# Kernel optimization log

Measured on AMD Instinct MI355X. Metric: run time of the kernel, lower is better.

## Reference

```python
import jax, jax.numpy as jnp
import numpy as np

N = 100_000      # nodes
E = 1_600_000    # edges (avg degree 16)
IN, H, C = 32, 32, 8


def setup_inputs() -> dict:
    key = jax.random.key(0)
    k0, k1, k2, k3, k4 = jax.random.split(key, 5)
    in_feat = jax.random.normal(k0, (N, IN), jnp.float32)
    src = jax.random.randint(k1, (E,), 0, N, dtype=jnp.int32)
    dst = jax.random.randint(k2, (E,), 0, N, dtype=jnp.int32)
    # Glorot-ish init for the two GraphConv weights, zero bias (DGL default)
    W1 = jax.random.normal(k3, (IN, H), jnp.float32) * (1.0 / np.sqrt(IN))
    b1 = jnp.zeros((H,), jnp.float32)
    W2 = jax.random.normal(k4, (H, C), jnp.float32) * (1.0 / np.sqrt(H))
    b2 = jnp.zeros((C,), jnp.float32)
    return {"in_feat": in_feat, "src": src, "dst": dst,
            "W1": W1, "b1": b1, "W2": W2, "b2": b2}


def _graph_conv(x, src, dst, W, b):
    """DGL GraphConv, norm='both': D_in^{-1/2} A D_out^{-1/2} (x W) + b."""
    ones = jnp.ones((src.shape[0],), x.dtype)
    deg_out = jnp.clip(jax.ops.segment_sum(ones, src, num_segments=N), 1.0)  # [N]
    deg_in = jnp.clip(jax.ops.segment_sum(ones, dst, num_segments=N), 1.0)   # [N]
    # weight applied before aggregation (DGL does this when in>=out; same math)
    h = (x @ W) * jax.lax.rsqrt(deg_out)[:, None]                # [N, out]
    agg = jax.ops.segment_sum(h[src], dst, num_segments=N)       # gather + scatter-add
    return agg * jax.lax.rsqrt(deg_in)[:, None] + b


def reference(in_feat, src, dst, W1, b1, W2, b2):
    h = jax.nn.relu(_graph_conv(in_feat, src, dst, W1, b1))
    h = _graph_conv(h, src, dst, W2, b2)
    return jnp.mean(h, axis=0)  # mean-pool readout over all nodes -> [C]
```

## Files before the change

kernel.cpp:

```cpp
#include <hip/hip_runtime.h>
#include <hip/hip_fp16.h>

#define NN 100000
#define NE 1600000
#define INF 32
#define HF 32
#define CF 8

#define SH1 11
#define BN1 2048
#define NB1 49
#define CAP1 36864
#define BNODE 64
#define NBF (NB1 * 32)
#define CAPF 1280
#define CHUNK 2048
#define NBLK_BIN ((NE + CHUNK - 1) / CHUNK)

__global__ void zero_kernel(uint4* __restrict__ p, int n16) {
    int i = blockIdx.x * blockDim.x + threadIdx.x;
    if (i < n16) p[i] = make_uint4(0u, 0u, 0u, 0u);
}

__global__ void __launch_bounds__(256) bin_coarse_kernel(
        const int* __restrict__ src, const int* __restrict__ dst,
        int* __restrict__ gcur_d, int* __restrict__ gcur_s,
        unsigned int* __restrict__ bins_d, unsigned int* __restrict__ bins_s) {
    __shared__ int cnt_d[4][NB1], base_d[4][NB1], cnt_s[4][NB1], base_s[4][NB1];
    const int tid = threadIdx.x;
    const int w = tid >> 6;
    for (int i = tid; i < 4 * NB1; i += 256) {
        (&cnt_d[0][0])[i] = 0; (&cnt_s[0][0])[i] = 0;
    }
    __syncthreads();
    int e0 = blockIdx.x * CHUNK;
    int e1 = min(e0 + CHUNK, NE);
    for (int e = e0 + tid; e < e1; e += 256) {
        atomicAdd(&cnt_d[w][dst[e] >> SH1], 1);
        atomicAdd(&cnt_s[w][src[e] >> SH1], 1);
    }
    __syncthreads();
    if (tid < NB1) {
        int c0 = cnt_d[0][tid], c1 = cnt_d[1][tid], c2 = cnt_d[2][tid], c3 = cnt_d[3][tid];
        int tot = c0 + c1 + c2 + c3;
        int b = tot ? atomicAdd(&gcur_d[tid], tot) : 0;
        base_d[0][tid] = b; base_d[1][tid] = b + c0;
        base_d[2][tid] = b + c0 + c1; base_d[3][tid] = b + c0 + c1 + c2;
        cnt_d[0][tid] = 0; cnt_d[1][tid] = 0; cnt_d[2][tid] = 0; cnt_d[3][tid] = 0;
        c0 = cnt_s[0][tid]; c1 = cnt_s[1][tid]; c2 = cnt_s[2][tid]; c3 = cnt_s[3][tid];
        tot = c0 + c1 + c2 + c3;
        b = tot ? atomicAdd(&gcur_s[tid], tot) : 0;
        base_s[0][tid] = b; base_s[1][tid] = b + c0;
        base_s[2][tid] = b + c0 + c1; base_s[3][tid] = b + c0 + c1 + c2;
        cnt_s[0][tid] = 0; cnt_s[1][tid] = 0; cnt_s[2][tid] = 0; cnt_s[3][tid] = 0;
    }
    __syncthreads();
    for (int e = e0 + tid; e < e1; e += 256) {
        int d = dst[e], s = src[e];
        int b = d >> SH1;
        int off = base_d[w][b] + atomicAdd(&cnt_d[w][b], 1);
        if (off < CAP1)
            bins_d[(size_t)b * CAP1 + off] = ((unsigned)(d & (BN1 - 1)) << 17) | (unsigned)s;
        b = s >> SH1;
        off = base_s[w][b] + atomicAdd(&cnt_s[w][b], 1);
        if (off < CAP1)
            bins_s[(size_t)b * CAP1 + off] = ((unsigned)(s & (BN1 - 1)) << 17) | (unsigned)d;
    }
}

__global__ void __launch_bounds__(256) bin_fine_kernel(
        const unsigned int* __restrict__ bins_d, const int* __restrict__ gcur_d,
        int* __restrict__ gcur_f, unsigned int* __restrict__ bins_f,
        int* __restrict__ deg_in) {
    __shared__ int cnt[8][32], base[8][32];
    __shared__ int ncnt[BN1];
    const int cb = blockIdx.x >> 4;
    const int sl = blockIdx.x & 15;
    const int tid = threadIdx.x;
    const int r = tid >> 5;
    (&cnt[0][0])[tid] = 0;
    for (int i = tid; i < BN1; i += 256) ncnt[i] = 0;
    __syncthreads();
    const int m = min(gcur_d[cb], CAP1);
    const int beg = (sl * m) >> 4;
    const int end = ((sl + 1) * m) >> 4;
    const unsigned int* bb = bins_d + (size_t)cb * CAP1;
    for (int j = beg + tid; j < end; j += 256) {
        int d10 = (int)(bb[j] >> 17);
        atomicAdd(&cnt[r][d10 >> 6], 1);
        atomicAdd(&ncnt[d10], 1);
    }
    __syncthreads();
    if (tid < 32) {
        int c[8], tot = 0;
        #pragma unroll
        for (int k = 0; k < 8; ++k) { c[k] = cnt[k][tid]; tot += c[k]; }
        int b = tot ? atomicAdd(&gcur_f[cb * 32 + tid], tot) : 0;
        #pragma unroll
        for (int k = 0; k < 8; ++k) { base[k][tid] = b; b += c[k]; cnt[k][tid] = 0; }
    }
    __syncthreads();
    for (int j = beg + tid; j < end; j += 256) {
        unsigned p = bb[j];
        int d10 = p >> 17;
        int f = d10 >> 6;
        int off = base[r][f] + atomicAdd(&cnt[r][f], 1);
        if (off < CAPF)
            bins_f[(size_t)(cb * 32 + f) * CAPF + off] =
                ((unsigned)(d10 & 63) << 17) | (p & 0x1FFFFu);
    }
    for (int i = tid; i < BN1; i += 256) {
        int c = ncnt[i];
        int n = cb * BN1 + i;
        if (c && n < NN) atomicAdd(&deg_in[n], c);
    }
}

__global__ void __launch_bounds__(256) srcside_kernel(
        const unsigned int* __restrict__ bins_s, const int* __restrict__ gcur_s,
        const int* __restrict__ deg_in,
        int* __restrict__ deg_out, float* __restrict__ wgt) {
    __shared__ int cnt[BN1];
    __shared__ float sw[BN1];
    const int cb = blockIdx.x >> 3;
    const int sl = blockIdx.x & 7;
    const int tid = threadIdx.x;
    for (int i = tid; i < BN1; i += 256) { cnt[i] = 0; sw[i] = 0.f; }
    __syncthreads();
    const int m = min(gcur_s[cb], CAP1);
    const int beg = (sl * m) >> 3;
    const int end = ((sl + 1) * m) >> 3;
    const unsigned int* bb = bins_s + (size_t)cb * CAP1;
    for (int j = beg + tid; j < end; j += 256) {
        unsigned p = bb[j];
        int local = p >> 17;
        int d = p & 0x1FFFF;
        float riv = rsqrtf(fmaxf((float)deg_in[d], 1.0f));
        atomicAdd(&cnt[local], 1);
        atomicAdd(&sw[local], riv);
    }
    __syncthreads();
    for (int i = tid; i < BN1; i += 256) {
        int c = cnt[i];
        int n = cb * BN1 + i;
        if (c && n < NN) {
            atomicAdd(&deg_out[n], c);
            atomicAdd(&wgt[n], sw[i]);
        }
    }
}

__global__ void xw1_kernel(const float* __restrict__ x, const float* __restrict__ W1,
                           const int* __restrict__ deg_out, unsigned int* __restrict__ h) {
    __shared__ float w[INF * HF];
    for (int i = threadIdx.x; i < INF * HF; i += blockDim.x) w[i] = W1[i];
    __syncthreads();
    int n = blockIdx.x * blockDim.x + threadIdx.x;
    if (n >= NN) return;

    float xr[INF];
    const float4* xp = (const float4*)(x + (size_t)n * INF);
    #pragma unroll
    for (int i = 0; i < INF / 4; ++i) {
        float4 v = xp[i];
        xr[4*i+0] = v.x; xr[4*i+1] = v.y; xr[4*i+2] = v.z; xr[4*i+3] = v.w;
    }
    float acc[HF];
    #pragma unroll
    for (int c = 0; c < HF; ++c) acc[c] = 0.0f;
    #pragma unroll
    for (int k = 0; k < INF; ++k) {
        float xv = xr[k];
        #pragma unroll
        for (int c = 0; c < HF; ++c) acc[c] = fmaf(xv, w[k * HF + c], acc[c]);
    }
    float rs = rsqrtf(fmaxf((float)deg_out[n], 1.0f));
    unsigned int pk[HF / 2];
    #pragma unroll
    for (int i = 0; i < HF / 2; ++i) {
        __half2 p = __floats2half2_rn(acc[2*i] * rs, acc[2*i+1] * rs);
        pk[i] = *(unsigned int*)&p;
    }
    uint4* hp = (uint4*)(h + (size_t)n * (HF / 2));
    #pragma unroll
    for (int i = 0; i < 4; ++i) {
        uint4 v;
        v.x = pk[4*i+0]; v.y = pk[4*i+1]; v.z = pk[4*i+2]; v.w = pk[4*i+3];
        hp[i] = v;
    }
}

__global__ void __launch_bounds__(256) gather_kernel(
        const unsigned int* __restrict__ bins, const int* __restrict__ gcur,
        const unsigned int* __restrict__ h, const int* __restrict__ deg_out,
        const float* __restrict__ wgt, const float* __restrict__ b1,
        float* __restrict__ v) {
    __shared__ int s_cnt[BNODE];
    __shared__ int s_start[BNODE];
    __shared__ int s_cur[BNODE];
    __shared__ int s_src[CAPF];
    __shared__ float vl[32];
    const int tid = threadIdx.x;
    const int b = blockIdx.x;
    const int m = min(gcur[b], CAPF);
    const unsigned int* bb = bins + (size_t)b * CAPF;

    if (tid < BNODE) s_cnt[tid] = 0;
    __syncthreads();
    for (int j = tid; j < m; j += 256) atomicAdd(&s_cnt[bb[j] >> 17], 1);
    __syncthreads();
    if (tid < 64) {
        int c = s_cnt[tid];
        int sc = c;
        #pragma unroll
        for (int off = 1; off < 64; off <<= 1) {
            int t = __shfl_up(sc, off, 64);
            if (tid >= off) sc += t;
        }
        s_start[tid] = sc - c;
        s_cur[tid] = sc - c;
    }
    __syncthreads();
    for (int j = tid; j < m; j += 256) {
        unsigned p = bb[j];
        int pos = atomicAdd(&s_cur[p >> 17], 1);
        s_src[pos] = (int)(p & 0x1FFFF);
    }
    __syncthreads();

    const int lane4 = tid & 3;
    const int g = tid >> 2;
    float b1r[8];
    #pragma unroll
    for (int c = 0; c < 8; ++c) b1r[c] = b1[lane4 * 8 + c];
    float vacc[8] = {0.f,0.f,0.f,0.f,0.f,0.f,0.f,0.f};

    #define ACC8(q) { float2 f0_ = __half22float2(*(__half2*)&(q).x); \
                      float2 f1_ = __half22float2(*(__half2*)&(q).y); \
                      float2 f2_ = __half22float2(*(__half2*)&(q).z); \
                      float2 f3_ = __half22float2(*(__half2*)&(q).w); \
                      a[0]+=f0_.x; a[1]+=f0_.y; a[2]+=f1_.x; a[3]+=f1_.y; \
                      a[4]+=f2_.x; a[5]+=f2_.y; a[6]+=f3_.x; a[7]+=f3_.y; }

    int n = b * BNODE + g;
    if (n < NN) {
        int beg = s_start[g];
        int cn = s_cnt[g];
        int end = beg + cn;
        float a[8] = {0.f,0.f,0.f,0.f,0.f,0.f,0.f,0.f};
        int j = beg;
        for (; j + 8 <= end; j += 8) {
            int t0 = s_src[j+0], t1 = s_src[j+1], t2 = s_src[j+2], t3 = s_src[j+3];
            int t4 = s_src[j+4], t5 = s_src[j+5], t6 = s_src[j+6], t7 = s_src[j+7];
            uint4 q0 = *(const uint4*)(h + (size_t)t0 * 16 + lane4 * 4);
            uint4 q1 = *(const uint4*)(h + (size_t)t1 * 16 + lane4 * 4);
            uint4 q2 = *(const uint4*)(h + (size_t)t2 * 16 + lane4 * 4);
            uint4 q3 = *(const uint4*)(h + (size_t)t3 * 16 + lane4 * 4);
            uint4 q4 = *(const uint4*)(h + (size_t)t4 * 16 + lane4 * 4);
            uint4 q5 = *(const uint4*)(h + (size_t)t5 * 16 + lane4 * 4);
            uint4 q6 = *(const uint4*)(h + (size_t)t6 * 16 + lane4 * 4);
            uint4 q7 = *(const uint4*)(h + (size_t)t7 * 16 + lane4 * 4);
            ACC8(q0) ACC8(q1) ACC8(q2) ACC8(q3)
            ACC8(q4) ACC8(q5) ACC8(q6) ACC8(q7)
        }
        for (; j + 4 <= end; j += 4) {
            int t0 = s_src[j+0], t1 = s_src[j+1], t2 = s_src[j+2], t3 = s_src[j+3];
            uint4 q0 = *(const uint4*)(h + (size_t)t0 * 16 + lane4 * 4);
            uint4 q1 = *(const uint4*)(h + (size_t)t1 * 16 + lane4 * 4);
            uint4 q2 = *(const uint4*)(h + (size_t)t2 * 16 + lane4 * 4);
            uint4 q3 = *(const uint4*)(h + (size_t)t3 * 16 + lane4 * 4);
            ACC8(q0) ACC8(q1) ACC8(q2) ACC8(q3)
        }
        for (; j < end; ++j) {
            int t0 = s_src[j];
            uint4 q0 = *(const uint4*)(h + (size_t)t0 * 16 + lane4 * 4);
            ACC8(q0)
        }
        float rs_in  = rsqrtf(fmaxf((float)cn, 1.0f));
        float rs_out = rsqrtf(fmaxf((float)deg_out[n], 1.0f));
        float alpha = rs_out * wgt[n];
        #pragma unroll
        for (int c = 0; c < 8; ++c)
            vacc[c] += alpha * fmaxf(fmaf(a[c], rs_in, b1r[c]), 0.f);
    }
    #undef ACC8

    #pragma unroll
    for (int c = 0; c < 8; ++c) {
        vacc[c] += __shfl_xor(vacc[c], 4, 64);
        vacc[c] += __shfl_xor(vacc[c], 8, 64);
        vacc[c] += __shfl_xor(vacc[c], 16, 64);
        vacc[c] += __shfl_xor(vacc[c], 32, 64);
    }
    if (tid < 32) vl[tid] = 0.f;
    __syncthreads();
    if ((tid & 63) < 4) {
        #pragma unroll
        for (int c = 0; c < 8; ++c) atomicAdd(&vl[lane4 * 8 + c], vacc[c]);
    }
    __syncthreads();
    if (tid < 32) atomicAdd(&v[tid], vl[tid]);
}

__global__ void final_kernel(const float* __restrict__ v, const float* __restrict__ W2,
                             const float* __restrict__ b2, float* __restrict__ out) {
    int c = threadIdx.x;
    if (c < CF) {
        float s = 0.f;
        #pragma unroll
        for (int k = 0; k < HF; ++k) s = fmaf(v[k], W2[k * CF + c], s);
        out[c] = s * (1.0f / NN) + b2[c];
    }
}

static inline size_t align256(size_t x) { return (x + 255) & ~(size_t)255; }

extern "C" void kernel_launch(void* const* d_in, const int* in_sizes, int n_in,
                              void* d_out, int out_size, void* d_ws, size_t ws_size,
                              hipStream_t stream) {
    const float* x   = (const float*)d_in[0];
    const int*   src = (const int*)  d_in[1];
    const int*   dst = (const int*)  d_in[2];
    const float* W1  = (const float*)d_in[3];
    const float* b1  = (const float*)d_in[4];
    const float* W2  = (const float*)d_in[5];
    const float* b2  = (const float*)d_in[6];
    float* out = (float*)d_out;

    char* base = (char*)d_ws;
    size_t off = 0;
    int*   gcur_d  = (int*)(base + off);   off = align256(off + NB1 * 4);
    int*   gcur_s  = (int*)(base + off);   off = align256(off + NB1 * 4);
    int*   gcur_f  = (int*)(base + off);   off = align256(off + NBF * 4);
    float* v       = (float*)(base + off); off = align256(off + 32 * 4);
    int*   deg_in  = (int*)(base + off);   off = align256(off + NN * 4);
    int*   deg_out = (int*)(base + off);   off = align256(off + NN * 4);
    float* wgt     = (float*)(base + off); off = align256(off + NN * 4);
    size_t zero_bytes = off;
    unsigned int* h      = (unsigned int*)(base + off); off = align256(off + (size_t)NN * 16 * 4);
    unsigned int* bins_d = (unsigned int*)(base + off); off = align256(off + (size_t)NB1 * CAP1 * 4);
    unsigned int* bins_s = (unsigned int*)(base + off); off = align256(off + (size_t)NB1 * CAP1 * 4);
    unsigned int* bins_f = (unsigned int*)(base + off); off = align256(off + (size_t)NBF * CAPF * 4);

    const int B = 256;
    int n16 = (int)(zero_bytes / 16);
    zero_kernel<<<(n16 + B - 1) / B, B, 0, stream>>>((uint4*)base, n16);

    bin_coarse_kernel<<<NBLK_BIN, B, 0, stream>>>(src, dst, gcur_d, gcur_s, bins_d, bins_s);
    bin_fine_kernel<<<NB1 * 16, B, 0, stream>>>(bins_d, gcur_d, gcur_f, bins_f, deg_in);
    srcside_kernel<<<NB1 * 8, B, 0, stream>>>(bins_s, gcur_s, deg_in, deg_out, wgt);
    xw1_kernel<<<(NN + B - 1) / B, B, 0, stream>>>(x, W1, deg_out, h);
    gather_kernel<<<NBF, B, 0, stream>>>(bins_f, gcur_f, h, deg_out, wgt, b1, v);
    final_kernel<<<1, 64, 0, stream>>>(v, W2, b2, out);
}
```

Before: 123.6 us.

## Fuse all pipeline stages into one cooperative persistent kernel with grid syncs

Merges the zero, binning, fine-binning, source-side degree, XW1, gather and final kernels into a single cooperative kernel launched with a persistent grid sized from occupancy. Each stage loops over its original block indices and stages are separated by grid-wide syncs. The aim is to remove the launch overhead and gaps between seven small kernels. In exchange, occupancy is limited by the shared-memory and register needs of the merged kernel, stages that had more blocks than the grid now loop, and grid syncs have their own cost. The old multi-kernel path remains as a fallback if the cooperative launch fails.

Result: no change. 123.8 us (+0.2%).

```diff
diff --git a/kernel.cpp b/kernel.cpp
--- a/kernel.cpp
+++ b/kernel.cpp
@@ -1,5 +1,7 @@
 #include <hip/hip_runtime.h>
 #include <hip/hip_fp16.h>
+#include <hip/hip_cooperative_groups.h>
+namespace cg = cooperative_groups;
 
 #define NN 100000
 #define NE 1600000
@@ -16,6 +18,313 @@
 #define CAPF 1280
 #define CHUNK 2048
 #define NBLK_BIN ((NE + CHUNK - 1) / CHUNK)
+
+#define SMEM_INTS 4096
+
+__global__ void __launch_bounds__(256) mega_kernel(
+        const float* __restrict__ x, const int* __restrict__ src, const int* __restrict__ dst,
+        const float* __restrict__ W1, const float* __restrict__ b1,
+        const float* __restrict__ W2, const float* __restrict__ b2,
+        float* __restrict__ out,
+        int* gcur_d, int* gcur_s, int* gcur_f, float* v,
+        int* deg_in, int* deg_out, float* wgt,
+        unsigned int* h, unsigned int* bins_d, unsigned int* bins_s, unsigned int* bins_f,
+        uint4* zbase, int n16) {
+    cg::grid_group gg = cg::this_grid();
+    __shared__ __align__(16) int smem[SMEM_INTS];
+    const int tid = threadIdx.x;
+    const int nb = gridDim.x;
+    const int gsz = nb * 256;
+
+    for (int i = blockIdx.x * 256 + tid; i < n16; i += gsz)
+        zbase[i] = make_uint4(0u, 0u, 0u, 0u);
+    __threadfence();
+    gg.sync();
+
+    {
+        int* cnt_d  = smem;
+        int* base_d = smem + 196;
+        int* cnt_s  = smem + 392;
+        int* base_s = smem + 588;
+        const int w = tid >> 6;
+        for (int c = blockIdx.x; c < NBLK_BIN; c += nb) {
+            for (int i = tid; i < 196; i += 256) { cnt_d[i] = 0; cnt_s[i] = 0; }
+            __syncthreads();
+            int e0 = c * CHUNK, e1 = min(e0 + CHUNK, NE);
+            for (int e = e0 + tid; e < e1; e += 256) {
+                atomicAdd(&cnt_d[w * 49 + (dst[e] >> SH1)], 1);
+                atomicAdd(&cnt_s[w * 49 + (src[e] >> SH1)], 1);
+            }
+            __syncthreads();
+            if (tid < NB1) {
+                int c0 = cnt_d[tid], c1 = cnt_d[49 + tid], c2 = cnt_d[98 + tid], c3 = cnt_d[147 + tid];
+                int tot = c0 + c1 + c2 + c3;
+                int b = tot ? atomicAdd(&gcur_d[tid], tot) : 0;
+                base_d[tid] = b; base_d[49 + tid] = b + c0;
+                base_d[98 + tid] = b + c0 + c1; base_d[147 + tid] = b + c0 + c1 + c2;
+                cnt_d[tid] = 0; cnt_d[49 + tid] = 0; cnt_d[98 + tid] = 0; cnt_d[147 + tid] = 0;
+                c0 = cnt_s[tid]; c1 = cnt_s[49 + tid]; c2 = cnt_s[98 + tid]; c3 = cnt_s[147 + tid];
+                tot = c0 + c1 + c2 + c3;
+                b = tot ? atomicAdd(&gcur_s[tid], tot) : 0;
+                base_s[tid] = b; base_s[49 + tid] = b + c0;
+                base_s[98 + tid] = b + c0 + c1; base_s[147 + tid] = b + c0 + c1 + c2;
+                cnt_s[tid] = 0; cnt_s[49 + tid] = 0; cnt_s[98 + tid] = 0; cnt_s[147 + tid] = 0;
+            }
+            __syncthreads();
+            for (int e = e0 + tid; e < e1; e += 256) {
+                int d = dst[e], s = src[e];
+                int b = d >> SH1;
+                int off = base_d[w * 49 + b] + atomicAdd(&cnt_d[w * 49 + b], 1);
+                if (off < CAP1)
+                    bins_d[(size_t)b * CAP1 + off] = ((unsigned)(d & (BN1 - 1)) << 17) | (unsigned)s;
+                b = s >> SH1;
+                off = base_s[w * 49 + b] + atomicAdd(&cnt_s[w * 49 + b], 1);
+                if (off < CAP1)
+                    bins_s[(size_t)b * CAP1 + off] = ((unsigned)(s & (BN1 - 1)) << 17) | (unsigned)d;
+            }
+            __syncthreads();
+        }
+    }
+    __threadfence();
+    gg.sync();
+
+    {
+        int* cnt  = smem;
+        int* base = smem + 256;
+        int* ncnt = smem + 512;
+        const int r = tid >> 5;
+        for (int t = blockIdx.x; t < NB1 * 16; t += nb) {
+            const int cb = t >> 4, sl = t & 15;
+            cnt[tid] = 0;
+            for (int i = tid; i < BN1; i += 256) ncnt[i] = 0;
+            __syncthreads();
+            const int m = min(gcur_d[cb], CAP1);
+            const int beg = (sl * m) >> 4, end = ((sl + 1) * m) >> 4;
+            const unsigned int* bb = bins_d + (size_t)cb * CAP1;
+            for (int j = beg + tid; j < end; j += 256) {
+                int d10 = (int)(bb[j] >> 17);
+                atomicAdd(&cnt[r * 32 + (d10 >> 6)], 1);
+                atomicAdd(&ncnt[d10], 1);
+            }
+            __syncthreads();
+            if (tid < 32) {
+                int cc[8], tot = 0;
+                #pragma unroll
+                for (int k = 0; k < 8; ++k) { cc[k] = cnt[k * 32 + tid]; tot += cc[k]; }
+                int b = tot ? atomicAdd(&gcur_f[cb * 32 + tid], tot) : 0;
+                #pragma unroll
+                for (int k = 0; k < 8; ++k) { base[k * 32 + tid] = b; b += cc[k]; cnt[k * 32 + tid] = 0; }
+            }
+            __syncthreads();
+            for (int j = beg + tid; j < end; j += 256) {
+                unsigned p = bb[j];
+                int d10 = p >> 17;
+                int f = d10 >> 6;
+                int off = base[r * 32 + f] + atomicAdd(&cnt[r * 32 + f], 1);
+                if (off < CAPF)
+                    bins_f[(size_t)(cb * 32 + f) * CAPF + off] =
+                        ((unsigned)(d10 & 63) << 17) | (p & 0x1FFFFu);
+            }
+            for (int i = tid; i < BN1; i += 256) {
+                int c = ncnt[i];
+                int n = cb * BN1 + i;
+                if (c && n < NN) atomicAdd(&deg_in[n], c);
+            }
+            __syncthreads();
+        }
+    }
+    __threadfence();
+    gg.sync();
+
+    {
+        int* cnt = smem;
+        float* sw = (float*)(smem + 2048);
+        for (int t = blockIdx.x; t < NB1 * 8; t += nb) {
+            const int cb = t >> 3, sl = t & 7;
+            for (int i = tid; i < BN1; i += 256) { cnt[i] = 0; sw[i] = 0.f; }
+            __syncthreads();
+            const int m = min(gcur_s[cb], CAP1);
+            const int beg = (sl * m) >> 3, end = ((sl + 1) * m) >> 3;
+            const unsigned int* bb = bins_s + (size_t)cb * CAP1;
+            for (int j = beg + tid; j < end; j += 256) {
+                unsigned p = bb[j];
+                int local = p >> 17;
+                int d = p & 0x1FFFF;
+                float riv = rsqrtf(fmaxf((float)deg_in[d], 1.0f));
+                atomicAdd(&cnt[local], 1);
+                atomicAdd(&sw[local], riv);
+            }
+            __syncthreads();
+            for (int i = tid; i < BN1; i += 256) {
+                int c = cnt[i];
+                int n = cb * BN1 + i;
+                if (c && n < NN) {
+                    atomicAdd(&deg_out[n], c);
+                    atomicAdd(&wgt[n], sw[i]);
+                }
+            }
+            __syncthreads();
+        }
+    }
+    __threadfence();
+    gg.sync();
+
+    {
+        float* w = (float*)smem;
+        for (int i = tid; i < INF * HF; i += 256) w[i] = W1[i];
+        __syncthreads();
+        for (int n = blockIdx.x * 256 + tid; n < NN; n += gsz) {
+            float xr[INF];
+            const float4* xp = (const float4*)(x + (size_t)n * INF);
+            #pragma unroll
+            for (int i = 0; i < INF / 4; ++i) {
+                float4 vv = xp[i];
+                xr[4*i+0] = vv.x; xr[4*i+1] = vv.y; xr[4*i+2] = vv.z; xr[4*i+3] = vv.w;
+            }
+            float acc[HF];
+            #pragma unroll
+            for (int c = 0; c < HF; ++c) acc[c] = 0.0f;
+            #pragma unroll
+            for (int k = 0; k < INF; ++k) {
+                float xv = xr[k];
+                #pragma unroll
+                for (int c = 0; c < HF; ++c) acc[c] = fmaf(xv, w[k * HF + c], acc[c]);
+            }
+            float rs = rsqrtf(fmaxf((float)deg_out[n], 1.0f));
+            unsigned int pk[HF / 2];
+            #pragma unroll
+            for (int i = 0; i < HF / 2; ++i) {
+                __half2 p = __floats2half2_rn(acc[2*i] * rs, acc[2*i+1] * rs);
+                pk[i] = *(unsigned int*)&p;
+            }
+            uint4* hp = (uint4*)(h + (size_t)n * (HF / 2));
+            #pragma unroll
+            for (int i = 0; i < 4; ++i) {
+                uint4 vv;
+                vv.x = pk[4*i+0]; vv.y = pk[4*i+1]; vv.z = pk[4*i+2]; vv.w = pk[4*i+3];
+                hp[i] = vv;
+            }
+        }
+    }
+    __threadfence();
+    gg.sync();
+
+    {
+        int* s_cnt   = smem;
+        int* s_start = smem + 64;
+        int* s_cur   = smem + 128;
+        int* s_src   = smem + 192;
+        float* vl    = (float*)(smem + 1472);
+        const int lane4 = tid & 3;
+        const int g = tid >> 2;
+        for (int bk = blockIdx.x; bk < NBF; bk += nb) {
+            const int m = min(gcur_f[bk], CAPF);
+            const unsigned int* bb = bins_f + (size_t)bk * CAPF;
+            if (tid < BNODE) s_cnt[tid] = 0;
+            __syncthreads();
+            for (int j = tid; j < m; j += 256) atomicAdd(&s_cnt[bb[j] >> 17], 1);
+            __syncthreads();
+            if (tid < 64) {
+                int c = s_cnt[tid];
+                int sc = c;
+                #pragma unroll
+                for (int off = 1; off < 64; off <<= 1) {
+                    int t = __shfl_up(sc, off, 64);
+                    if (tid >= off) sc += t;
+                }
+                s_start[tid] = sc - c;
+                s_cur[tid] = sc - c;
+            }
+            __syncthreads();
+            for (int j = tid; j < m; j += 256) {
+                unsigned p = bb[j];
+                int pos = atomicAdd(&s_cur[p >> 17], 1);
+                s_src[pos] = (int)(p & 0x1FFFF);
+            }
+            __syncthreads();
+
+            float b1r[8];
+            #pragma unroll
+            for (int c = 0; c < 8; ++c) b1r[c] = b1[lane4 * 8 + c];
+            float vacc[8] = {0.f,0.f,0.f,0.f,0.f,0.f,0.f,0.f};
+
+            #define ACC8(q) { float2 f0_ = __half22float2(*(__half2*)&(q).x); \
+                              float2 f1_ = __half22float2(*(__half2*)&(q).y); \
+                              float2 f2_ = __half22float2(*(__half2*)&(q).z); \
+                              float2 f3_ = __half22float2(*(__half2*)&(q).w); \
+                              a[0]+=f0_.x; a[1]+=f0_.y; a[2]+=f1_.x; a[3]+=f1_.y; \
+                              a[4]+=f2_.x; a[5]+=f2_.y; a[6]+=f3_.x; a[7]+=f3_.y; }
+
+            int n = bk * BNODE + g;
+            if (n < NN) {
+                int beg = s_start[g];
+                int cn = s_cnt[g];
+                int end = beg + cn;
+                float a[8] = {0.f,0.f,0.f,0.f,0.f,0.f,0.f,0.f};
+                int j = beg;
+                for (; j + 8 <= end; j += 8) {
+                    int t0 = s_src[j+0], t1 = s_src[j+1], t2 = s_src[j+2], t3 = s_src[j+3];
+                    int t4 = s_src[j+4], t5 = s_src[j+5], t6 = s_src[j+6], t7 = s_src[j+7];
+                    uint4 q0 = *(const uint4*)(h + (size_t)t0 * 16 + lane4 * 4);
+                    uint4 q1 = *(const uint4*)(h + (size_t)t1 * 16 + lane4 * 4);
+                    uint4 q2 = *(const uint4*)(h + (size_t)t2 * 16 + lane4 * 4);
+                    uint4 q3 = *(const uint4*)(h + (size_t)t3 * 16 + lane4 * 4);
+                    uint4 q4 = *(const uint4*)(h + (size_t)t4 * 16 + lane4 * 4);
+                    uint4 q5 = *(const uint4*)(h + (size_t)t5 * 16 + lane4 * 4);
+                    uint4 q6 = *(const uint4*)(h + (size_t)t6 * 16 + lane4 * 4);
+                    uint4 q7 = *(const uint4*)(h + (size_t)t7 * 16 + lane4 * 4);
+                    ACC8(q0) ACC8(q1) ACC8(q2) ACC8(q3)
+                    ACC8(q4) ACC8(q5) ACC8(q6) ACC8(q7)
+                }
+                for (; j + 4 <= end; j += 4) {
+                    int t0 = s_src[j+0], t1 = s_src[j+1], t2 = s_src[j+2], t3 = s_src[j+3];
+                    uint4 q0 = *(const uint4*)(h + (size_t)t0 * 16 + lane4 * 4);
+                    uint4 q1 = *(const uint4*)(h + (size_t)t1 * 16 + lane4 * 4);
+                    uint4 q2 = *(const uint4*)(h + (size_t)t2 * 16 + lane4 * 4);
+                    uint4 q3 = *(const uint4*)(h + (size_t)t3 * 16 + lane4 * 4);
+                    ACC8(q0) ACC8(q1) ACC8(q2) ACC8(q3)
+                }
+                for (; j < end; ++j) {
+                    int t0 = s_src[j];
+                    uint4 q0 = *(const uint4*)(h + (size_t)t0 * 16 + lane4 * 4);
+                    ACC8(q0)
+                }
+                float rs_in  = rsqrtf(fmaxf((float)cn, 1.0f));
+                float rs_out = rsqrtf(fmaxf((float)deg_out[n], 1.0f));
+                float alpha = rs_out * wgt[n];
+                #pragma unroll
+                for (int c = 0; c < 8; ++c)
+                    vacc[c] += alpha * fmaxf(fmaf(a[c], rs_in, b1r[c]), 0.f);
+            }
+            #undef ACC8
+
+            #pragma unroll
+            for (int c = 0; c < 8; ++c) {
+                vacc[c] += __shfl_xor(vacc[c], 4, 64);
+                vacc[c] += __shfl_xor(vacc[c], 8, 64);
+                vacc[c] += __shfl_xor(vacc[c], 16, 64);
+                vacc[c] += __shfl_xor(vacc[c], 32, 64);
+            }
+            if (tid < 32) vl[tid] = 0.f;
+            __syncthreads();
+            if ((tid & 63) < 4) {
+                #pragma unroll
+                for (int c = 0; c < 8; ++c) atomicAdd(&vl[lane4 * 8 + c], vacc[c]);
+            }
+            __syncthreads();
+            if (tid < 32) atomicAdd(&v[tid], vl[tid]);
+        }
+    }
+    __threadfence();
+    gg.sync();
+
+    if (blockIdx.x == 0 && tid < CF) {
+        float s = 0.f;
+        #pragma unroll
+        for (int k = 0; k < HF; ++k) s = fmaf(v[k], W2[k * CF + tid], s);
+        out[tid] = s * (1.0f / NN) + b2[tid];
+    }
+}
 
 __global__ void zero_kernel(uint4* __restrict__ p, int n16) {
     int i = blockIdx.x * blockDim.x + threadIdx.x;
@@ -313,7 +622,7 @@
     }
 }
 
-static inline size_t align256(size_t x) { return (x + 255) & ~(size_t)255; }
+static inline size_t align256(size_t xx) { return (xx + 255) & ~(size_t)255; }
 
 extern "C" void kernel_launch(void* const* d_in, const int* in_sizes, int n_in,
                               void* d_out, int out_size, void* d_ws, size_t ws_size,
@@ -342,10 +651,35 @@
     unsigned int* bins_s = (unsigned int*)(base + off); off = align256(off + (size_t)NB1 * CAP1 * 4);
     unsigned int* bins_f = (unsigned int*)(base + off); off = align256(off + (size_t)NBF * CAPF * 4);
 
+    uint4* zbase = (uint4*)base;
+    int n16 = (int)(zero_bytes / 16);
     const int B = 256;
-    int n16 = (int)(zero_bytes / 16);
-    zero_kernel<<<(n16 + B - 1) / B, B, 0, stream>>>((uint4*)base, n16);
-
+
+    hipError_t cerr = hipErrorUnknown;
+    int dev = 0;
+    (void)hipGetDevice(&dev);
+    int numCU = 0;
+    if (hipDeviceGetAttribute(&numCU, hipDeviceAttributeMultiprocessorCount, dev) != hipSuccess || numCU <= 0)
+        numCU = 256;
+    int maxb = 0;
+    if (hipOccupancyMaxActiveBlocksPerMultiprocessor(&maxb, (const void*)mega_kernel, 256, 0) != hipSuccess)
+        maxb = 0;
+    if (maxb > 0) {
+        long long grid = (long long)maxb * numCU;
+        if (grid > NBF) grid = NBF;
+        void* args[] = { (void*)&x, (void*)&src, (void*)&dst, (void*)&W1, (void*)&b1,
+                         (void*)&W2, (void*)&b2, (void*)&out,
+                         (void*)&gcur_d, (void*)&gcur_s, (void*)&gcur_f, (void*)&v,
+                         (void*)&deg_in, (void*)&deg_out, (void*)&wgt,
+                         (void*)&h, (void*)&bins_d, (void*)&bins_s, (void*)&bins_f,
+                         (void*)&zbase, (void*)&n16 };
+        cerr = hipLaunchCooperativeKernel((const void*)mega_kernel, dim3((unsigned)grid),
+                                          dim3(256), args, 0, stream);
+    }
+    if (cerr == hipSuccess) return;
+
+    int blocks16 = (n16 + B - 1) / B;
+    zero_kernel<<<blocks16, B, 0, stream>>>(zbase, n16);
     bin_coarse_kernel<<<NBLK_BIN, B, 0, stream>>>(src, dst, gcur_d, gcur_s, bins_d, bins_s);
     bin_fine_kernel<<<NB1 * 16, B, 0, stream>>>(bins_d, gcur_d, gcur_f, bins_f, deg_in);
     srcside_kernel<<<NB1 * 8, B, 0, stream>>>(bins_s, gcur_s, deg_in, deg_out, wgt);
```
